# Kernel optimization log

Measured on AMD Instinct MI355X. Metric: run time of the kernel, lower is better.

The kernel has to match this reference:

```python
import jax, jax.numpy as jnp
import numpy as np

D_MODEL = 1024
N_HEADS = 16
HEAD_DIM = D_MODEL // N_HEADS
B, T = 4, 2048


def setup_inputs() -> dict:
    key = jax.random.key(0)
    ks = jax.random.split(key, 5)
    x = jax.random.normal(ks[0], (B, T, D_MODEL), dtype=jnp.float32)
    # causal mask; masked_fill(mask == 0, -inf) => attend where mask is True
    mask = jnp.tril(jnp.ones((T, T), dtype=bool))
    # parameters (torch Linear: y = x @ W.T + b); store already-transposed [in, out]
    s_in = 1.0 / np.sqrt(D_MODEL)
    Wqkv = jax.random.uniform(ks[1], (D_MODEL, 3 * D_MODEL), jnp.float32, -s_in, s_in)
    bqkv = jax.random.uniform(ks[2], (3 * D_MODEL,), jnp.float32, -s_in, s_in)
    Wout = jax.random.uniform(ks[3], (D_MODEL, D_MODEL), jnp.float32, -s_in, s_in)
    bout = jax.random.uniform(ks[4], (D_MODEL,), jnp.float32, -s_in, s_in)
    return {"x": x, "mask": mask, "Wqkv": Wqkv, "bqkv": bqkv, "Wout": Wout, "bout": bout}


def reference(x, mask, Wqkv, bqkv, Wout, bout):
    Bq, Tq, C = x.shape
    qkv = x @ Wqkv + bqkv                       # [B, T, 3C]
    q, k, v = jnp.split(qkv, 3, axis=-1)
    def split_heads(t):
        return t.reshape(Bq, Tq, N_HEADS, HEAD_DIM).transpose(0, 2, 1, 3)  # [B,H,T,d]
    q, k, v = split_heads(q), split_heads(k), split_heads(v)
    scale = 1.0 / np.sqrt(HEAD_DIM).astype(np.float32)
    att = jnp.einsum("bhqd,bhkd->bhqk", q, k) * scale  # [B,H,T,T]
    att = jnp.where(mask, att, -jnp.inf)
    att = jax.nn.softmax(att, axis=-1)
    out = jnp.einsum("bhqk,bhkd->bhqd", att, v)         # [B,H,T,d]
    out = out.transpose(0, 2, 1, 3).reshape(Bq, Tq, C)  # [B,T,C]
    return out @ Wout + bout
```

## Files before the change

kernel.cpp:

```cpp
#include <hip/hip_runtime.h>
#include <hip/hip_bf16.h>
#include <cstdint>
#include <cstddef>

#define DMODEL 1024
#define NHEADS 16
#define HDIM 64
#define BATCH 4
#define SEQ 2048
#define MROWS (BATCH*SEQ)
#define N3 (3*DMODEL)
#define BHCNT (BATCH*NHEADS)

typedef __attribute__((ext_vector_type(8))) short short8;
typedef __attribute__((ext_vector_type(4))) short short4v;
typedef __attribute__((ext_vector_type(4))) float f32x4;
typedef __attribute__((ext_vector_type(4))) unsigned int uint4v;

static __device__ __forceinline__ short f2bf(float f) {
  unsigned int u = __builtin_bit_cast(unsigned int, f);
  return (short)((u + 0x7fffu + ((u >> 16) & 1u)) >> 16);
}

static __device__ __forceinline__ unsigned int pack_bf16(float lo, float hi) {
  unsigned int r;
  asm("v_cvt_pk_bf16_f32 %0, %1, %2" : "=v"(r) : "v"(lo), "v"(hi));
  return r;
}

static __device__ __forceinline__ void permlane32_swap(unsigned int& a, unsigned int& b) {
  asm("v_permlane32_swap_b32 %0, %1" : "+v"(a), "+v"(b));
}
static __device__ __forceinline__ void permlane16_swap(unsigned int& a, unsigned int& b) {
  asm("v_permlane16_swap_b32 %0, %1" : "+v"(a), "+v"(b));
}

static __device__ __forceinline__ float fast_exp2(float x) {
#if __has_builtin(__builtin_amdgcn_exp2f)
  return __builtin_amdgcn_exp2f(x);
#else
  return exp2f(x);
#endif
}

static __device__ __forceinline__ void gload16(const void* g, void* l) {
  __builtin_amdgcn_global_load_lds(
      (const __attribute__((address_space(1))) unsigned int*)g,
      (__attribute__((address_space(3))) unsigned int*)l, 16, 0, 0);
}

__global__ __launch_bounds__(256) void cast_x_kernel(
    const float* __restrict__ in, short* __restrict__ out, int n) {
  int i = (blockIdx.x * 256 + threadIdx.x) * 4;
  if (i + 3 < n) {
    float4 v = *(const float4*)(in + i);
    short4v s;
    s[0] = f2bf(v.x); s[1] = f2bf(v.y); s[2] = f2bf(v.z); s[3] = f2bf(v.w);
    *(short4v*)(out + i) = s;
  }
}

__global__ __launch_bounds__(256) void transpose_cast_kernel(
    const float* __restrict__ in, short* __restrict__ out, int K, int N) {
  __shared__ float tile[32][33];
  int n0 = blockIdx.x * 32, k0 = blockIdx.y * 32;
  int tx = threadIdx.x, ty = threadIdx.y;
#pragma unroll
  for (int i = 0; i < 4; ++i)
    tile[ty + i * 8][tx] = in[(size_t)(k0 + ty + i * 8) * N + (n0 + tx)];
  __syncthreads();
#pragma unroll
  for (int i = 0; i < 4; ++i)
    out[(size_t)(n0 + ty + i * 8) * K + (k0 + tx)] = f2bf(tile[tx][ty + i * 8]);
}

template <int EPI>
__global__ __launch_bounds__(256, 2) void gemm128_kernel(
    const short* __restrict__ A, const short* __restrict__ Bt,
    const float* __restrict__ bias, float* __restrict__ foutp,
    short* __restrict__ q_out, short* __restrict__ k_out,
    short* __restrict__ v_out, int Mdim, int Ndim, int Kdim) {
  __shared__ __align__(16) short As[128 * 32];
  __shared__ __align__(16) short Bs[128 * 32];
  const int tid = threadIdx.x;
  const int lane = tid & 63;
  const int w = tid >> 6;
  const int wr = w >> 1, wc = w & 1;
  const int nwg = gridDim.x * gridDim.y;
  const int lin = blockIdx.y * gridDim.x + blockIdx.x;
  const int tile = (lin & 7) * (nwg >> 3) + (lin >> 3);
  const int row0 = (tile / gridDim.x) * 128;
  const int col0 = (tile % gridDim.x) * 128;
  const int lrow = lane & 15, lkg = lane >> 4;

  f32x4 acc[4][4];
#pragma unroll
  for (int i = 0; i < 4; ++i)
#pragma unroll
    for (int j = 0; j < 4; ++j) acc[i][j] = (f32x4){0.f, 0.f, 0.f, 0.f};

  const short* Ab = A + (size_t)row0 * Kdim;
  const short* Bb = Bt + (size_t)col0 * Kdim;
  const int sr = tid >> 2;
  const int sc = (tid & 3) * 8;

  for (int kt = 0; kt < Kdim; kt += 32) {
    gload16(Ab + (size_t)sr * Kdim + kt + sc, As + tid * 8);
    gload16(Ab + (size_t)(sr + 64) * Kdim + kt + sc, As + 2048 + tid * 8);
    gload16(Bb + (size_t)sr * Kdim + kt + sc, Bs + tid * 8);
    gload16(Bb + (size_t)(sr + 64) * Kdim + kt + sc, Bs + 2048 + tid * 8);
    __syncthreads();
    short8 af[4], bfr[4];
#pragma unroll
    for (int i = 0; i < 4; ++i)
      af[i] = *(const short8*)(As + (wr * 64 + i * 16 + lrow) * 32 + lkg * 8);
#pragma unroll
    for (int j = 0; j < 4; ++j)
      bfr[j] = *(const short8*)(Bs + (wc * 64 + j * 16 + lrow) * 32 + lkg * 8);
#pragma unroll
    for (int i = 0; i < 4; ++i)
#pragma unroll
      for (int j = 0; j < 4; ++j)
        acc[i][j] = __builtin_amdgcn_mfma_f32_16x16x32_bf16(af[i], bfr[j], acc[i][j], 0, 0, 0);
    __syncthreads();
  }

#pragma unroll
  for (int i = 0; i < 4; ++i) {
#pragma unroll
    for (int j = 0; j < 4; ++j) {
      const int gn = col0 + wc * 64 + j * 16 + lrow;
      const int gmb = row0 + wr * 64 + i * 16 + lkg * 4;
      float vr[4];
#pragma unroll
      for (int r = 0; r < 4; ++r) vr[r] = acc[i][j][r] + bias[gn];
      if (EPI == 0) {
        const int which = gn >> 10;
        const int hh = (gn >> 6) & 15;
        const int dd = gn & 63;
        const int b = gmb >> 11;
        const int tt0 = gmb & 2047;
        const size_t bh = (size_t)b * NHEADS + hh;
        if (which == 0) {
#pragma unroll
          for (int r = 0; r < 4; ++r)
            q_out[(bh * SEQ + tt0 + r) * HDIM + dd] = f2bf(vr[r] * 0.125f);
        } else if (which == 1) {
#pragma unroll
          for (int r = 0; r < 4; ++r)
            k_out[(bh * SEQ + tt0 + r) * HDIM + (dd ^ (((tt0 + r) & 7) << 3))] = f2bf(vr[r]);
        } else {
          short4v pk;
#pragma unroll
          for (int r = 0; r < 4; ++r) pk[r] = f2bf(vr[r]);
          *(short4v*)(v_out + (bh * HDIM + dd) * SEQ + (tt0 ^ ((dd & 7) << 3))) = pk;
        }
      } else {
#pragma unroll
        for (int r = 0; r < 4; ++r)
          foutp[(size_t)(gmb + r) * Ndim + gn] = vr[r];
      }
    }
  }
}

__global__ __launch_bounds__(256, 4) void attn_kernel(
    const short* __restrict__ qb, const short* __restrict__ kb,
    const short* __restrict__ vb, short* __restrict__ aout) {
  __shared__ __align__(16) short Ks2[2][64 * 64];
  __shared__ __align__(16) short Vs2[2][64 * 64];
  const int tid = threadIdx.x;
  const int lane = tid & 63;
  const int w = tid >> 6;
  const int lin = blockIdx.y * gridDim.x + blockIdx.x;
  const int tile = ((lin & 7) << 7) + (lin >> 3);
  const int bh = tile >> 4;
  const int qblk = 15 - (tile & 15);
  const int q0 = qblk * 128;
  const int qw0 = q0 + w * 32;
  const int lrow = lane & 15, lkg = lane >> 4;

  const short* kbase = kb + (size_t)bh * SEQ * HDIM;
  const short* vbase = vb + (size_t)bh * HDIM * SEQ;

  short8 qf[2][2];
#pragma unroll
  for (int rb = 0; rb < 2; ++rb) {
    const short* qrow = qb + ((size_t)bh * SEQ + qw0 + rb * 16 + lrow) * HDIM;
    qf[rb][0] = *(const short8*)(qrow + lkg * 8);
    qf[rb][1] = *(const short8*)(qrow + 32 + lkg * 8);
  }

  f32x4 o[2][4];
  float mr[2], lsum[2];
#pragma unroll
  for (int rb = 0; rb < 2; ++rb) {
#pragma unroll
    for (int g = 0; g < 4; ++g) o[rb][g] = (f32x4){0.f, 0.f, 0.f, 0.f};
    mr[rb] = -__builtin_inff();
    lsum[rb] = 0.f;
  }

  const int ntile = 2 * (qblk + 1);

  {
    short* Kd = Ks2[0]; short* Vd = Vs2[0];
    gload16(kbase + tid * 8, Kd + tid * 8);
    gload16(kbase + 2048 + tid * 8, Kd + 2048 + tid * 8);
    gload16(vbase + (size_t)(tid >> 3) * SEQ + (tid & 7) * 8, Vd + tid * 8);
    gload16(vbase + (size_t)((tid >> 3) + 32) * SEQ + (tid & 7) * 8, Vd + 2048 + tid * 8);
  }
  __syncthreads();

  int cur = 0;
  for (int it = 0; it < ntile; ++it) {
    const int kt = it * 64;
    if (it + 1 < ntile) {
      const int k2 = kt + 64;
      short* Kd = Ks2[cur ^ 1]; short* Vd = Vs2[cur ^ 1];
      gload16(kbase + (size_t)k2 * HDIM + tid * 8, Kd + tid * 8);
      gload16(kbase + (size_t)k2 * HDIM + 2048 + tid * 8, Kd + 2048 + tid * 8);
      gload16(vbase + (size_t)(tid >> 3) * SEQ + k2 + (tid & 7) * 8, Vd + tid * 8);
      gload16(vbase + (size_t)((tid >> 3) + 32) * SEQ + k2 + (tid & 7) * 8, Vd + 2048 + tid * 8);
    }
    if (kt <= qw0 + 31) {
      const short* Kc = Ks2[cur];
      const short* Vc = Vs2[cur];

      f32x4 s[2][4];
#pragma unroll
      for (int rb = 0; rb < 2; ++rb)
#pragma unroll
        for (int f = 0; f < 4; ++f) s[rb][f] = (f32x4){0.f, 0.f, 0.f, 0.f};

      __builtin_amdgcn_s_setprio(1);
#pragma unroll
      for (int c = 0; c < 2; ++c) {
#pragma unroll
        for (int f = 0; f < 4; ++f) {
          const int krow = f * 16 + lrow;
          const int kel = (c * 32 + lkg * 8) ^ ((krow & 7) << 3);
          short8 kf = *(const short8*)(Kc + krow * 64 + kel);
          s[0][f] = __builtin_amdgcn_mfma_f32_16x16x32_bf16(kf, qf[0][c], s[0][f], 0, 0, 0);
          s[1][f] = __builtin_amdgcn_mfma_f32_16x16x32_bf16(kf, qf[1][c], s[1][f], 0, 0, 0);
        }
      }
      __builtin_amdgcn_s_setprio(0);

      if (kt + 63 > qw0) {
#pragma unroll
        for (int rb = 0; rb < 2; ++rb) {
          const int qq = qw0 + rb * 16 + lrow;
#pragma unroll
          for (int f = 0; f < 4; ++f) {
            const int kg = kt + f * 16 + lkg * 4;
#pragma unroll
            for (int r = 0; r < 4; ++r)
              if (kg + r > qq) s[rb][f][r] = -__builtin_inff();
          }
        }
      }

      const float L2E = 1.44269504088896340736f;
      float al[2];
      unsigned int q32[2][4][2];
#pragma unroll
      for (int rb = 0; rb < 2; ++rb) {
        float pm = fmaxf(fmaxf(fmaxf(s[rb][0][0], s[rb][0][1]), fmaxf(s[rb][0][2], s[rb][0][3])),
                         fmaxf(fmaxf(s[rb][1][0], s[rb][1][1]), fmaxf(s[rb][1][2], s[rb][1][3])));
        pm = fmaxf(pm, fmaxf(fmaxf(fmaxf(s[rb][2][0], s[rb][2][1]), fmaxf(s[rb][2][2], s[rb][2][3])),
                             fmaxf(fmaxf(s[rb][3][0], s[rb][3][1]), fmaxf(s[rb][3][2], s[rb][3][3]))));
        pm = fmaxf(pm, __shfl_xor(pm, 16));
        pm = fmaxf(pm, __shfl_xor(pm, 32));
        const float mn = fmaxf(mr[rb], pm);
        al[rb] = fast_exp2((mr[rb] - mn) * L2E);
        mr[rb] = mn;
        float rs = 0.f;
#pragma unroll
        for (int f = 0; f < 4; ++f)
#pragma unroll
          for (int r = 0; r < 4; ++r) {
            const float p = fast_exp2((s[rb][f][r] - mn) * L2E);
            s[rb][f][r] = p;
            rs += p;
          }
        rs += __shfl_xor(rs, 16);
        rs += __shfl_xor(rs, 32);
        lsum[rb] = lsum[rb] * al[rb] + rs;
#pragma unroll
        for (int f = 0; f < 4; ++f) {
          q32[rb][f][0] = pack_bf16(s[rb][f][0], s[rb][f][1]);
          q32[rb][f][1] = pack_bf16(s[rb][f][2], s[rb][f][3]);
        }
      }

#pragma unroll
      for (int r = 0; r < 4; ++r) {
        const float a0 = __shfl(al[0], lkg * 4 + r, 16);
        const float a1 = __shfl(al[1], lkg * 4 + r, 16);
#pragma unroll
        for (int g = 0; g < 4; ++g) { o[0][g][r] *= a0; o[1][g][r] *= a1; }
      }

      __builtin_amdgcn_s_setprio(1);
#pragma unroll
      for (int c = 0; c < 2; ++c) {
        uint4v pw0, pw1;
#pragma unroll
        for (int h = 0; h < 2; ++h) {
          unsigned int a0 = q32[0][2 * c][h], b0 = q32[0][2 * c + 1][h];
          permlane32_swap(a0, b0);
          permlane16_swap(a0, b0);
          pw0[h] = a0; pw0[2 + h] = b0;
          unsigned int a1 = q32[1][2 * c][h], b1 = q32[1][2 * c + 1][h];
          permlane32_swap(a1, b1);
          permlane16_swap(a1, b1);
          pw1[h] = a1; pw1[2 + h] = b1;
        }
        const short8 pf0 = __builtin_bit_cast(short8, pw0);
        const short8 pf1 = __builtin_bit_cast(short8, pw1);
#pragma unroll
        for (int g = 0; g < 4; ++g) {
          const int vrow = g * 16 + lrow;
          const int vel = (c * 32 + lkg * 8) ^ ((vrow & 7) << 3);
          short8 vf = *(const short8*)(Vc + vrow * 64 + vel);
          o[0][g] = __builtin_amdgcn_mfma_f32_16x16x32_bf16(pf0, vf, o[0][g], 0, 0, 0);
          o[1][g] = __builtin_amdgcn_mfma_f32_16x16x32_bf16(pf1, vf, o[1][g], 0, 0, 0);
        }
      }
      __builtin_amdgcn_s_setprio(0);
    }
    __syncthreads();
    cur ^= 1;
  }

  const int b = bh >> 4, h = bh & 15;
  const float li0 = 1.0f / lsum[0];
  const float li1 = 1.0f / lsum[1];
#pragma unroll
  for (int r = 0; r < 4; ++r) {
    const float i0 = __shfl(li0, lkg * 4 + r, 16);
    const float i1 = __shfl(li1, lkg * 4 + r, 16);
    const int t0 = qw0 + lkg * 4 + r;
#pragma unroll
    for (int g = 0; g < 4; ++g) {
      aout[((size_t)b * SEQ + t0) * DMODEL + h * 64 + g * 16 + lrow] = f2bf(o[0][g][r] * i0);
      aout[((size_t)b * SEQ + t0 + 16) * DMODEL + h * 64 + g * 16 + lrow] = f2bf(o[1][g][r] * i1);
    }
  }
}

extern "C" void kernel_launch(void* const* d_in, const int* in_sizes, int n_in,
                              void* d_out, int out_size, void* d_ws, size_t ws_size,
                              hipStream_t stream) {
  const float* x = (const float*)d_in[0];
  const float* Wqkv = (const float*)d_in[2];
  const float* bqkv = (const float*)d_in[3];
  const float* Wout = (const float*)d_in[4];
  const float* bout = (const float*)d_in[5];

  char* ws = (char*)d_ws;
  short* xb    = (short*)(ws + 0);
  short* wqkvT = (short*)(ws + 16777216);
  short* woutT = (short*)(ws + 23068672);
  short* qbuf  = (short*)(ws + 25165824);
  short* kbuf  = (short*)(ws + 41943040);
  short* vbuf  = (short*)(ws + 58720256);
  short* abuf  = (short*)(ws + 75497472);

  cast_x_kernel<<<(MROWS * DMODEL) / 4 / 256, 256, 0, stream>>>(x, xb, MROWS * DMODEL);
  transpose_cast_kernel<<<dim3(N3 / 32, DMODEL / 32), dim3(32, 8), 0, stream>>>(
      Wqkv, wqkvT, DMODEL, N3);
  transpose_cast_kernel<<<dim3(DMODEL / 32, DMODEL / 32), dim3(32, 8), 0, stream>>>(
      Wout, woutT, DMODEL, DMODEL);
  gemm128_kernel<0><<<dim3(N3 / 128, MROWS / 128), 256, 0, stream>>>(
      xb, wqkvT, bqkv, nullptr, qbuf, kbuf, vbuf, MROWS, N3, DMODEL);
  attn_kernel<<<dim3(SEQ / 128, BHCNT), 256, 0, stream>>>(qbuf, kbuf, vbuf, abuf);
  gemm128_kernel<1><<<dim3(DMODEL / 128, MROWS / 128), 256, 0, stream>>>(
      abuf, woutT, bout, (float*)d_out, nullptr, nullptr, nullptr, MROWS, DMODEL, DMODEL);
}
```

Baseline: 309.3 us.

## Shrink attention tiles to 64 queries with 128-thread single-buffered blocks

The attention kernel now uses 64-query tiles handled by 2 waves per block, doubling the grid so causal work is split more finely across CUs. The double-buffered K/V prefetch is replaced by a single LDS buffer loaded synchronously each iteration, bracketed by two barriers. The per-wave causal skip check is no longer needed, because every tile is now valid for both waves. The online-softmax rescale of the output accumulators and running sum is skipped when no row maximum grows anywhere in the wave. The trade-off is finer load balance and less LDS per block against the loss of overlap between global loads and MFMA work.

```diff
diff --git a/kernel.cpp b/kernel.cpp
--- a/kernel.cpp
+++ b/kernel.cpp
@@ -164,19 +164,19 @@
   }
 }
 
-__global__ __launch_bounds__(256, 4) void attn_kernel(
+__global__ __launch_bounds__(128, 5) void attn_kernel(
     const short* __restrict__ qb, const short* __restrict__ kb,
     const short* __restrict__ vb, short* __restrict__ aout) {
-  __shared__ __align__(16) short Ks2[2][64 * 64];
-  __shared__ __align__(16) short Vs2[2][64 * 64];
+  __shared__ __align__(16) short Ks[64 * 64];
+  __shared__ __align__(16) short Vs[64 * 64];
   const int tid = threadIdx.x;
   const int lane = tid & 63;
   const int w = tid >> 6;
   const int lin = blockIdx.y * gridDim.x + blockIdx.x;
-  const int tile = ((lin & 7) << 7) + (lin >> 3);
-  const int bh = tile >> 4;
-  const int qblk = 15 - (tile & 15);
-  const int q0 = qblk * 128;
+  const int tile = ((lin & 7) << 8) + (lin >> 3);
+  const int bh = tile >> 5;
+  const int qblk = 31 - (tile & 31);
+  const int q0 = qblk * 64;
   const int qw0 = q0 + w * 32;
   const int lrow = lane & 15, lkg = lane >> 4;
 
@@ -201,137 +201,133 @@
     lsum[rb] = 0.f;
   }
 
-  const int ntile = 2 * (qblk + 1);
-
-  {
-    short* Kd = Ks2[0]; short* Vd = Vs2[0];
-    gload16(kbase + tid * 8, Kd + tid * 8);
-    gload16(kbase + 2048 + tid * 8, Kd + 2048 + tid * 8);
-    gload16(vbase + (size_t)(tid >> 3) * SEQ + (tid & 7) * 8, Vd + tid * 8);
-    gload16(vbase + (size_t)((tid >> 3) + 32) * SEQ + (tid & 7) * 8, Vd + 2048 + tid * 8);
-  }
-  __syncthreads();
-
-  int cur = 0;
+  const int ntile = qblk + 1;
+
   for (int it = 0; it < ntile; ++it) {
     const int kt = it * 64;
-    if (it + 1 < ntile) {
-      const int k2 = kt + 64;
-      short* Kd = Ks2[cur ^ 1]; short* Vd = Vs2[cur ^ 1];
-      gload16(kbase + (size_t)k2 * HDIM + tid * 8, Kd + tid * 8);
-      gload16(kbase + (size_t)k2 * HDIM + 2048 + tid * 8, Kd + 2048 + tid * 8);
-      gload16(vbase + (size_t)(tid >> 3) * SEQ + k2 + (tid & 7) * 8, Vd + tid * 8);
-      gload16(vbase + (size_t)((tid >> 3) + 32) * SEQ + k2 + (tid & 7) * 8, Vd + 2048 + tid * 8);
-    }
-    if (kt <= qw0 + 31) {
-      const short* Kc = Ks2[cur];
-      const short* Vc = Vs2[cur];
-
-      f32x4 s[2][4];
-#pragma unroll
-      for (int rb = 0; rb < 2; ++rb)
-#pragma unroll
-        for (int f = 0; f < 4; ++f) s[rb][f] = (f32x4){0.f, 0.f, 0.f, 0.f};
-
-      __builtin_amdgcn_s_setprio(1);
-#pragma unroll
-      for (int c = 0; c < 2; ++c) {
+    __syncthreads();
+#pragma unroll
+    for (int i = 0; i < 4; ++i)
+      gload16(kbase + (size_t)kt * HDIM + i * 1024 + tid * 8, Ks + i * 1024 + tid * 8);
+#pragma unroll
+    for (int i = 0; i < 4; ++i)
+      gload16(vbase + (size_t)(16 * i + (tid >> 3)) * SEQ + kt + (tid & 7) * 8,
+              Vs + (16 * i + (tid >> 3)) * 64 + (tid & 7) * 8);
+    __syncthreads();
+
+    f32x4 s[2][4];
+#pragma unroll
+    for (int rb = 0; rb < 2; ++rb)
+#pragma unroll
+      for (int f = 0; f < 4; ++f) s[rb][f] = (f32x4){0.f, 0.f, 0.f, 0.f};
+
+    __builtin_amdgcn_s_setprio(1);
+#pragma unroll
+    for (int c = 0; c < 2; ++c) {
+#pragma unroll
+      for (int f = 0; f < 4; ++f) {
+        const int krow = f * 16 + lrow;
+        const int kel = (c * 32 + lkg * 8) ^ ((krow & 7) << 3);
+        short8 kf = *(const short8*)(Ks + krow * 64 + kel);
+        s[0][f] = __builtin_amdgcn_mfma_f32_16x16x32_bf16(kf, qf[0][c], s[0][f], 0, 0, 0);
+        s[1][f] = __builtin_amdgcn_mfma_f32_16x16x32_bf16(kf, qf[1][c], s[1][f], 0, 0, 0);
+      }
+    }
+    __builtin_amdgcn_s_setprio(0);
+
+    if (kt + 63 > qw0) {
+#pragma unroll
+      for (int rb = 0; rb < 2; ++rb) {
+        const int qq = qw0 + rb * 16 + lrow;
 #pragma unroll
         for (int f = 0; f < 4; ++f) {
-          const int krow = f * 16 + lrow;
-          const int kel = (c * 32 + lkg * 8) ^ ((krow & 7) << 3);
-          short8 kf = *(const short8*)(Kc + krow * 64 + kel);
-          s[0][f] = __builtin_amdgcn_mfma_f32_16x16x32_bf16(kf, qf[0][c], s[0][f], 0, 0, 0);
-          s[1][f] = __builtin_amdgcn_mfma_f32_16x16x32_bf16(kf, qf[1][c], s[1][f], 0, 0, 0);
+          const int kg = kt + f * 16 + lkg * 4;
+#pragma unroll
+          for (int r = 0; r < 4; ++r)
+            if (kg + r > qq) s[rb][f][r] = -__builtin_inff();
         }
       }
-      __builtin_amdgcn_s_setprio(0);
-
-      if (kt + 63 > qw0) {
-#pragma unroll
-        for (int rb = 0; rb < 2; ++rb) {
-          const int qq = qw0 + rb * 16 + lrow;
-#pragma unroll
-          for (int f = 0; f < 4; ++f) {
-            const int kg = kt + f * 16 + lkg * 4;
-#pragma unroll
-            for (int r = 0; r < 4; ++r)
-              if (kg + r > qq) s[rb][f][r] = -__builtin_inff();
-          }
+    }
+
+    const float L2E = 1.44269504088896340736f;
+    float pm[2];
+#pragma unroll
+    for (int rb = 0; rb < 2; ++rb) {
+      float p = fmaxf(fmaxf(fmaxf(s[rb][0][0], s[rb][0][1]), fmaxf(s[rb][0][2], s[rb][0][3])),
+                      fmaxf(fmaxf(s[rb][1][0], s[rb][1][1]), fmaxf(s[rb][1][2], s[rb][1][3])));
+      p = fmaxf(p, fmaxf(fmaxf(fmaxf(s[rb][2][0], s[rb][2][1]), fmaxf(s[rb][2][2], s[rb][2][3])),
+                         fmaxf(fmaxf(s[rb][3][0], s[rb][3][1]), fmaxf(s[rb][3][2], s[rb][3][3]))));
+      p = fmaxf(p, __shfl_xor(p, 16));
+      p = fmaxf(p, __shfl_xor(p, 32));
+      pm[rb] = p;
+    }
+    const float mn0 = fmaxf(mr[0], pm[0]);
+    const float mn1 = fmaxf(mr[1], pm[1]);
+    if (!__all(pm[0] <= mr[0] && pm[1] <= mr[1])) {
+      const float a0 = fast_exp2((mr[0] - mn0) * L2E);
+      const float a1 = fast_exp2((mr[1] - mn1) * L2E);
+      lsum[0] *= a0;
+      lsum[1] *= a1;
+#pragma unroll
+      for (int r = 0; r < 4; ++r) {
+        const float s0 = __shfl(a0, lkg * 4 + r, 16);
+        const float s1 = __shfl(a1, lkg * 4 + r, 16);
+#pragma unroll
+        for (int g = 0; g < 4; ++g) { o[0][g][r] *= s0; o[1][g][r] *= s1; }
+      }
+    }
+    mr[0] = mn0; mr[1] = mn1;
+
+    unsigned int q32[2][4][2];
+#pragma unroll
+    for (int rb = 0; rb < 2; ++rb) {
+      const float mn = rb ? mn1 : mn0;
+      float rs = 0.f;
+#pragma unroll
+      for (int f = 0; f < 4; ++f)
+#pragma unroll
+        for (int r = 0; r < 4; ++r) {
+          const float p = fast_exp2((s[rb][f][r] - mn) * L2E);
+          s[rb][f][r] = p;
+          rs += p;
         }
-      }
-
-      const float L2E = 1.44269504088896340736f;
-      float al[2];
-      unsigned int q32[2][4][2];
-#pragma unroll
-      for (int rb = 0; rb < 2; ++rb) {
-        float pm = fmaxf(fmaxf(fmaxf(s[rb][0][0], s[rb][0][1]), fmaxf(s[rb][0][2], s[rb][0][3])),
-                         fmaxf(fmaxf(s[rb][1][0], s[rb][1][1]), fmaxf(s[rb][1][2], s[rb][1][3])));
-        pm = fmaxf(pm, fmaxf(fmaxf(fmaxf(s[rb][2][0], s[rb][2][1]), fmaxf(s[rb][2][2], s[rb][2][3])),
-                             fmaxf(fmaxf(s[rb][3][0], s[rb][3][1]), fmaxf(s[rb][3][2], s[rb][3][3]))));
-        pm = fmaxf(pm, __shfl_xor(pm, 16));
-        pm = fmaxf(pm, __shfl_xor(pm, 32));
-        const float mn = fmaxf(mr[rb], pm);
-        al[rb] = fast_exp2((mr[rb] - mn) * L2E);
-        mr[rb] = mn;
-        float rs = 0.f;
-#pragma unroll
-        for (int f = 0; f < 4; ++f)
-#pragma unroll
-          for (int r = 0; r < 4; ++r) {
-            const float p = fast_exp2((s[rb][f][r] - mn) * L2E);
-            s[rb][f][r] = p;
-            rs += p;
-          }
-        rs += __shfl_xor(rs, 16);
-        rs += __shfl_xor(rs, 32);
-        lsum[rb] = lsum[rb] * al[rb] + rs;
-#pragma unroll
-        for (int f = 0; f < 4; ++f) {
-          q32[rb][f][0] = pack_bf16(s[rb][f][0], s[rb][f][1]);
-          q32[rb][f][1] = pack_bf16(s[rb][f][2], s[rb][f][3]);
-        }
-      }
-
-#pragma unroll
-      for (int r = 0; r < 4; ++r) {
-        const float a0 = __shfl(al[0], lkg * 4 + r, 16);
-        const float a1 = __shfl(al[1], lkg * 4 + r, 16);
-#pragma unroll
-        for (int g = 0; g < 4; ++g) { o[0][g][r] *= a0; o[1][g][r] *= a1; }
-      }
-
-      __builtin_amdgcn_s_setprio(1);
-#pragma unroll
-      for (int c = 0; c < 2; ++c) {
-        uint4v pw0, pw1;
-#pragma unroll
-        for (int h = 0; h < 2; ++h) {
-          unsigned int a0 = q32[0][2 * c][h], b0 = q32[0][2 * c + 1][h];
-          permlane32_swap(a0, b0);
-          permlane16_swap(a0, b0);
-          pw0[h] = a0; pw0[2 + h] = b0;
-          unsigned int a1 = q32[1][2 * c][h], b1 = q32[1][2 * c + 1][h];
-          permlane32_swap(a1, b1);
-          permlane16_swap(a1, b1);
-          pw1[h] = a1; pw1[2 + h] = b1;
-        }
-        const short8 pf0 = __builtin_bit_cast(short8, pw0);
-        const short8 pf1 = __builtin_bit_cast(short8, pw1);
-#pragma unroll
-        for (int g = 0; g < 4; ++g) {
-          const int vrow = g * 16 + lrow;
-          const int vel = (c * 32 + lkg * 8) ^ ((vrow & 7) << 3);
-          short8 vf = *(const short8*)(Vc + vrow * 64 + vel);
-          o[0][g] = __builtin_amdgcn_mfma_f32_16x16x32_bf16(pf0, vf, o[0][g], 0, 0, 0);
-          o[1][g] = __builtin_amdgcn_mfma_f32_16x16x32_bf16(pf1, vf, o[1][g], 0, 0, 0);
-        }
-      }
-      __builtin_amdgcn_s_setprio(0);
-    }
-    __syncthreads();
-    cur ^= 1;
+      rs += __shfl_xor(rs, 16);
+      rs += __shfl_xor(rs, 32);
+      lsum[rb] += rs;
+#pragma unroll
+      for (int f = 0; f < 4; ++f) {
+        q32[rb][f][0] = pack_bf16(s[rb][f][0], s[rb][f][1]);
+        q32[rb][f][1] = pack_bf16(s[rb][f][2], s[rb][f][3]);
+      }
+    }
+
+    __builtin_amdgcn_s_setprio(1);
+#pragma unroll
+    for (int c = 0; c < 2; ++c) {
+      uint4v pw0, pw1;
+#pragma unroll
+      for (int h = 0; h < 2; ++h) {
+        unsigned int a0 = q32[0][2 * c][h], b0 = q32[0][2 * c + 1][h];
+        permlane32_swap(a0, b0);
+        permlane16_swap(a0, b0);
+        pw0[h] = a0; pw0[2 + h] = b0;
+        unsigned int a1 = q32[1][2 * c][h], b1 = q32[1][2 * c + 1][h];
+        permlane32_swap(a1, b1);
+        permlane16_swap(a1, b1);
+        pw1[h] = a1; pw1[2 + h] = b1;
+      }
+      const short8 pf0 = __builtin_bit_cast(short8, pw0);
+      const short8 pf1 = __builtin_bit_cast(short8, pw1);
+#pragma unroll
+      for (int g = 0; g < 4; ++g) {
+        const int vrow = g * 16 + lrow;
+        const int vel = (c * 32 + lkg * 8) ^ ((vrow & 7) << 3);
+        short8 vf = *(const short8*)(Vs + vrow * 64 + vel);
+        o[0][g] = __builtin_amdgcn_mfma_f32_16x16x32_bf16(pf0, vf, o[0][g], 0, 0, 0);
+        o[1][g] = __builtin_amdgcn_mfma_f32_16x16x32_bf16(pf1, vf, o[1][g], 0, 0, 0);
+      }
+    }
+    __builtin_amdgcn_s_setprio(0);
   }
 
   const int b = bh >> 4, h = bh & 15;
@@ -375,7 +371,7 @@
       Wout, woutT, DMODEL, DMODEL);
   gemm128_kernel<0><<<dim3(N3 / 128, MROWS / 128), 256, 0, stream>>>(
       xb, wqkvT, bqkv, nullptr, qbuf, kbuf, vbuf, MROWS, N3, DMODEL);
-  attn_kernel<<<dim3(SEQ / 128, BHCNT), 256, 0, stream>>>(qbuf, kbuf, vbuf, abuf);
+  attn_kernel<<<dim3(SEQ / 64, BHCNT), 128, 0, stream>>>(qbuf, kbuf, vbuf, abuf);
   gemm128_kernel<1><<<dim3(DMODEL / 128, MROWS / 128), 256, 0, stream>>>(
       abuf, woutT, bout, (float*)d_out, nullptr, nullptr, nullptr, MROWS, DMODEL, DMODEL);
 }
```

Measured after the change: 410.8 us. 32.8% more time.
